# Kernel tuning notes

Hardware: AMD Instinct MI355X
Metric: run time of the kernel (lower is better)

The kernel has to match this reference:

```python
import jax, jax.numpy as jnp
import numpy as np
import itertools

KH = KW = 3
N_NZ = 5
K_OUT = 126  # C(9,5) -> all patterns, matches capped n_kernels
C_IN = 128


def setup_inputs() -> dict:
    key = jax.random.key(0)
    k1, k2 = jax.random.split(key)
    inputs = jax.random.normal(k1, (32, 112, 112, C_IN), dtype=jnp.float32)
    # sparse_kernel: (n_non_zero, in_channels, kernels), glorot-ish scale
    scale = (2.0 / (N_NZ * C_IN + K_OUT)) ** 0.5
    sparse_kernel = jax.random.normal(k2, (N_NZ, C_IN, K_OUT), dtype=jnp.float32) * scale
    bias = jnp.zeros((K_OUT,), dtype=jnp.float32)
    # deterministic unique sparsity patterns: all C(9,5) flat-position combos
    patterns = jnp.asarray(
        np.array(list(itertools.combinations(range(KH * KW), N_NZ)), dtype=np.int32)
    )  # (K_OUT, N_NZ) flat positions in [0, 9)
    return {"inputs": inputs, "sparse_kernel": sparse_kernel, "bias": bias, "patterns": patterns}


def reference(inputs, sparse_kernel, bias, patterns):
    k_out = patterns.shape[0]
    c_in = sparse_kernel.shape[1]
    kk = jnp.arange(k_out)[:, None]  # (K,1) broadcasts against (K,N)
    # scatter: dense_flat[pos, :, k] = sparse_kernel[n, :, k]
    updates = jnp.transpose(sparse_kernel, (2, 0, 1))  # (K, N, Cin)
    dense_flat = jnp.zeros((KH * KW, c_in, k_out), dtype=inputs.dtype)
    dense_flat = dense_flat.at[patterns, :, kk].set(updates)
    dense_kernel = dense_flat.reshape(KH, KW, c_in, k_out)
    out = jax.lax.conv_general_dilated(
        inputs, dense_kernel, window_strides=(1, 1), padding="SAME",
        dimension_numbers=("NHWC", "HWIO", "NHWC"))
    return jax.nn.relu(out + bias)
```

## Files before the change

### kernel.cpp

```cpp
#include <hip/hip_runtime.h>


typedef __attribute__((ext_vector_type(8))) __bf16 bf16x8;
typedef __attribute__((ext_vector_type(4))) float f32x4;

__device__ __forceinline__ unsigned short f2bf(float f) {
  unsigned int u = __builtin_bit_cast(unsigned int, f);
  u += 0x7fffu + ((u >> 16) & 1u);
  return (unsigned short)(u >> 16);
}

__global__ __launch_bounds__(256) void build_B(const float* __restrict__ sk,
                                               const int* __restrict__ patterns,
                                               unsigned short* __restrict__ Bws) {
  int idx = blockIdx.x * 256 + threadIdx.x;
  if (idx >= 9 * 128 * 128) return;
  int c = idx & 127;
  int n = (idx >> 7) & 127;
  int p = idx >> 14;
  float v = 0.f;
  if (n < 126) {
#pragma unroll
    for (int j = 0; j < 5; ++j)
      if (patterns[n * 5 + j] == p) v = sk[(j * 128 + c) * 126 + n];
  }
  int cc = c >> 5, cl = c & 31;
  Bws[(((p * 4 + cc) * 128) + n) * 32 + cl] = f2bf(v);
}

__global__ __launch_bounds__(256, 2) void conv_main(const float* __restrict__ in,
                                                    const unsigned short* __restrict__ Bws,
                                                    const float* __restrict__ bias,
                                                    float* __restrict__ out) {
  __shared__ unsigned short Alds[2 * 4 * 342 * 8];

  const int tid = threadIdx.x;
  const int bid = ((blockIdx.x & 7) * 448) + (blockIdx.x >> 3);
  const int nimg = bid / 112;
  const int y = bid - nimg * 112;
  const int lane = tid & 63;
  const int w = tid >> 6;
  const int quad = lane >> 4;
  const int lrow = lane & 15;

  const float* inb = in + (size_t)nimg * 112 * 112 * 128;

  f32x4 acc[7][2];
#pragma unroll
  for (int mt = 0; mt < 7; ++mt) { acc[mt][0] = (f32x4)0.f; acc[mt][1] = (f32x4)0.f; }

  float4 pf[11];
  auto loadA = [&](int cc) {
#pragma unroll
    for (int it = 0; it < 11; ++it) {
      int i = tid + it * 256;
      float4 v = make_float4(0.f, 0.f, 0.f, 0.f);
      if (i < 2736) {
        int c4 = i & 7;
        int rest = i >> 3;
        int r = rest / 114;
        int hx = rest - r * 114;
        int gy = y + r - 1;
        int gx = hx - 1;
        if ((unsigned)gy < 112u && (unsigned)gx < 112u)
          v = *(const float4*)(inb + ((size_t)gy * 112 + gx) * 128 + cc * 32 + c4 * 4);
      }
      pf[it] = v;
    }
  };
  auto writeA = [&](int b) {
#pragma unroll
    for (int it = 0; it < 11; ++it) {
      int i = tid + it * 256;
      if (i < 2736) {
        int c4 = i & 7;
        int rest = i >> 3;
        int q = c4 >> 1, h = c4 & 1;
        ushort4 s;
        s.x = f2bf(pf[it].x); s.y = f2bf(pf[it].y);
        s.z = f2bf(pf[it].z); s.w = f2bf(pf[it].w);
        *(ushort4*)&Alds[(((b * 4 + q) * 342) + rest) * 8 + h * 4] = s;
      }
    }
  };

  loadA(0);
  writeA(0);
  __syncthreads();

#pragma unroll 1
  for (int cc = 0; cc < 4; ++cc) {
    const int cur = cc & 1;
    bf16x8 b[9][2];
#pragma unroll
    for (int p = 0; p < 9; ++p)
#pragma unroll
      for (int j = 0; j < 2; ++j)
        b[p][j] = *(const bf16x8*)(Bws +
            (((size_t)(p * 4 + cc) * 128 + w * 32 + j * 16 + lrow) * 32 + quad * 8));

    if (cc < 3) loadA(cc + 1);

    const unsigned short* Ab = &Alds[(size_t)(cur * 4 + quad) * 2736];
#pragma unroll
    for (int p = 0; p < 9; ++p) {
      const int r = p / 3;
      const int px = p - r * 3;
      const int abase = (r * 114 + px + lrow) * 8;
#pragma unroll
      for (int mt = 0; mt < 7; ++mt) {
        bf16x8 a = *(const bf16x8*)&Ab[abase + mt * 128];
        acc[mt][0] = __builtin_amdgcn_mfma_f32_16x16x32_bf16(a, b[p][0], acc[mt][0], 0, 0, 0);
        acc[mt][1] = __builtin_amdgcn_mfma_f32_16x16x32_bf16(a, b[p][1], acc[mt][1], 0, 0, 0);
      }
    }

    if (cc < 3) {
      writeA(cur ^ 1);
      __syncthreads();
    }
  }

  const int k0 = w * 32 + lrow;
  const int k1 = k0 + 16;
  const float bv0 = bias[k0 < 126 ? k0 : 125];
  const float bv1 = bias[k1 < 126 ? k1 : 125];
  float* outrow = out + ((size_t)(nimg * 112 + y)) * 112 * 126;
#pragma unroll
  for (int mt = 0; mt < 7; ++mt) {
#pragma unroll
    for (int rg = 0; rg < 4; ++rg) {
      int x = mt * 16 + quad * 4 + rg;
      float* o = outrow + (size_t)x * 126;
      if (k0 < 126) { float v = acc[mt][0][rg] + bv0; o[k0] = v > 0.f ? v : 0.f; }
      if (k1 < 126) { float v = acc[mt][1][rg] + bv1; o[k1] = v > 0.f ? v : 0.f; }
    }
  }
}

extern "C" void kernel_launch(void* const* d_in, const int* in_sizes, int n_in,
                              void* d_out, int out_size, void* d_ws, size_t ws_size,
                              hipStream_t stream) {
  const float* in = (const float*)d_in[0];
  const float* sk = (const float*)d_in[1];
  const float* bias = (const float*)d_in[2];
  const int* patterns = (const int*)d_in[3];
  float* out = (float*)d_out;
  unsigned short* Bws = (unsigned short*)d_ws;

  build_B<<<dim3(576), dim3(256), 0, stream>>>(sk, patterns, Bws);
  conv_main<<<dim3(32 * 112), dim3(256), 0, stream>>>(in, Bws, bias, out);
}
```

Before: 433.7 us.

## Precompute padded bf16 input rows and stage them into LDS with async copies

Adds a pre-pass kernel that converts the fp32 NHWC input into padded, channel-chunk-blocked bf16 rows in workspace. The main conv kernel then fills LDS with direct global-to-LDS 16-byte async loads from three neighbour rows, using a zero row for image borders. This removes the per-block fp32 load, conversion and LDS write, and the kernel now targets three blocks per SM. The cost is an extra pass that reads the full input and writes a bf16 copy, plus a memset. The old kernel is kept as a fallback when the workspace is too small.

```diff
diff --git a/kernel.cpp b/kernel.cpp
--- a/kernel.cpp
+++ b/kernel.cpp
@@ -3,12 +3,25 @@
 
 typedef __attribute__((ext_vector_type(8))) __bf16 bf16x8;
 typedef __attribute__((ext_vector_type(4))) float f32x4;
+typedef __attribute__((ext_vector_type(8))) unsigned short ushort8;
 
 __device__ __forceinline__ unsigned short f2bf(float f) {
   unsigned int u = __builtin_bit_cast(unsigned int, f);
   u += 0x7fffu + ((u >> 16) & 1u);
   return (unsigned short)(u >> 16);
 }
+
+__device__ __forceinline__ void async_copy16(void* lds, const void* g) {
+  __builtin_amdgcn_global_load_lds(
+      (const __attribute__((address_space(1))) unsigned int*)g,
+      (__attribute__((address_space(3))) unsigned int*)lds, 16, 0, 0);
+}
+
+#define BWS_BYTES 294912
+#define ROW_BYTES 29184
+#define ROW_USH   14592
+#define AIN_BYTES (3584LL * ROW_BYTES)
+#define WS_NEED   ((size_t)BWS_BYTES + (size_t)AIN_BYTES + (size_t)ROW_BYTES)
 
 __global__ __launch_bounds__(256) void build_B(const float* __restrict__ sk,
                                                const int* __restrict__ patterns,
@@ -28,10 +41,127 @@
   Bws[(((p * 4 + cc) * 128) + n) * 32 + cl] = f2bf(v);
 }
 
-__global__ __launch_bounds__(256, 2) void conv_main(const float* __restrict__ in,
+__global__ __launch_bounds__(256) void conv_pre(const float* __restrict__ in,
+                                                unsigned short* __restrict__ Ain) {
+  const int bid = ((blockIdx.x & 7) * 448) + (blockIdx.x >> 3);
+  const float* inrow = in + (size_t)bid * 112 * 128;
+  unsigned short* orow = Ain + (size_t)bid * ROW_USH;
+  const int tid = threadIdx.x;
+#pragma unroll
+  for (int it = 0; it < 8; ++it) {
+    int j = tid + it * 256;
+    if (j < 1824) {
+      int px = j >> 4;
+      int ccq = j & 15;
+      int gx = px - 1;
+      ushort8 s = (ushort8)0;
+      if ((unsigned)gx < 112u) {
+        const float* p = inrow + (size_t)gx * 128 + ccq * 8;
+        float4 a = *(const float4*)p;
+        float4 b = *(const float4*)(p + 4);
+        s[0] = f2bf(a.x); s[1] = f2bf(a.y); s[2] = f2bf(a.z); s[3] = f2bf(a.w);
+        s[4] = f2bf(b.x); s[5] = f2bf(b.y); s[6] = f2bf(b.z); s[7] = f2bf(b.w);
+      }
+      int cc = ccq >> 2, q = ccq & 3;
+      *(ushort8*)(orow + cc * 3648 + q * 912 + px * 8) = s;
+    }
+  }
+}
+
+__global__ __launch_bounds__(256, 3) void conv_main(const unsigned short* __restrict__ Ain,
+                                                    const unsigned short* __restrict__ zp,
                                                     const unsigned short* __restrict__ Bws,
                                                     const float* __restrict__ bias,
                                                     float* __restrict__ out) {
+  __shared__ unsigned short Alds[2 * 1536 * 8];
+
+  const int tid = threadIdx.x;
+  const int bid = ((blockIdx.x & 7) * 448) + (blockIdx.x >> 3);
+  const int nimg = bid / 112;
+  const int y = bid - nimg * 112;
+  const int lane = tid & 63;
+  const int w = tid >> 6;
+  const int quad = lane >> 4;
+  const int lrow = lane & 15;
+
+  const unsigned short* rp0;
+  const unsigned short* rp1 = Ain + (size_t)bid * ROW_USH;
+  const unsigned short* rp2;
+  rp0 = (y > 0)   ? (rp1 - ROW_USH) : zp;
+  rp2 = (y < 111) ? (rp1 + ROW_USH) : zp;
+
+  f32x4 acc[7][2];
+#pragma unroll
+  for (int mt = 0; mt < 7; ++mt) { acc[mt][0] = (f32x4)0.f; acc[mt][1] = (f32x4)0.f; }
+
+  auto stage = [&](int cc, int buf) {
+    const unsigned short* c0 = rp0 + cc * 3648;
+    const unsigned short* c1 = rp1 + cc * 3648;
+    const unsigned short* c2 = rp2 + cc * 3648;
+#pragma unroll
+    for (int it = 0; it < 6; ++it) {
+      int i = tid + it * 256;
+      bool b1 = (i >= 456), b2 = (i >= 912);
+      int rem = i - (b2 ? 912 : (b1 ? 456 : 0));
+      const unsigned short* base = b2 ? c2 : (b1 ? c1 : c0);
+      const unsigned short* src = (i < 1368) ? (base + rem * 8) : zp;
+      async_copy16((void*)&Alds[(size_t)buf * 12288 + (size_t)i * 8], (const void*)src);
+    }
+  };
+
+  stage(0, 0);
+  __syncthreads();
+
+#pragma unroll 1
+  for (int cc = 0; cc < 4; ++cc) {
+    const int buf = cc & 1;
+    bf16x8 b[9][2];
+#pragma unroll
+    for (int p = 0; p < 9; ++p)
+#pragma unroll
+      for (int j = 0; j < 2; ++j)
+        b[p][j] = *(const bf16x8*)(Bws +
+            (((size_t)(p * 4 + cc) * 128 + w * 32 + j * 16 + lrow) * 32 + quad * 8));
+
+    if (cc < 3) stage(cc + 1, buf ^ 1);
+
+#pragma unroll
+    for (int p = 0; p < 9; ++p) {
+      const int r = p / 3;
+      const int px = p - r * 3;
+      const int abase = buf * 12288 + r * 3648 + quad * 912 + (px + lrow) * 8;
+#pragma unroll
+      for (int mt = 0; mt < 7; ++mt) {
+        bf16x8 a = *(const bf16x8*)&Alds[abase + mt * 128];
+        acc[mt][0] = __builtin_amdgcn_mfma_f32_16x16x32_bf16(a, b[p][0], acc[mt][0], 0, 0, 0);
+        acc[mt][1] = __builtin_amdgcn_mfma_f32_16x16x32_bf16(a, b[p][1], acc[mt][1], 0, 0, 0);
+      }
+    }
+
+    if (cc < 3) __syncthreads();
+  }
+
+  const int k0 = w * 32 + lrow;
+  const int k1 = k0 + 16;
+  const float bv0 = bias[k0 < 126 ? k0 : 125];
+  const float bv1 = bias[k1 < 126 ? k1 : 125];
+  float* outrow = out + (size_t)bid * 112 * 126;
+#pragma unroll
+  for (int mt = 0; mt < 7; ++mt) {
+#pragma unroll
+    for (int rg = 0; rg < 4; ++rg) {
+      int x = mt * 16 + quad * 4 + rg;
+      float* o = outrow + (size_t)x * 126;
+      if (k0 < 126) { float v = acc[mt][0][rg] + bv0; o[k0] = v > 0.f ? v : 0.f; }
+      if (k1 < 126) { float v = acc[mt][1][rg] + bv1; o[k1] = v > 0.f ? v : 0.f; }
+    }
+  }
+}
+
+__global__ __launch_bounds__(256, 2) void conv_main_fb(const float* __restrict__ in,
+                                                       const unsigned short* __restrict__ Bws,
+                                                       const float* __restrict__ bias,
+                                                       float* __restrict__ out) {
   __shared__ unsigned short Alds[2 * 4 * 342 * 8];
 
   const int tid = threadIdx.x;
@@ -125,7 +255,7 @@
   const int k1 = k0 + 16;
   const float bv0 = bias[k0 < 126 ? k0 : 125];
   const float bv1 = bias[k1 < 126 ? k1 : 125];
-  float* outrow = out + ((size_t)(nimg * 112 + y)) * 112 * 126;
+  float* outrow = out + (size_t)bid * 112 * 126;
 #pragma unroll
   for (int mt = 0; mt < 7; ++mt) {
 #pragma unroll
@@ -149,5 +279,14 @@
   unsigned short* Bws = (unsigned short*)d_ws;
 
   build_B<<<dim3(576), dim3(256), 0, stream>>>(sk, patterns, Bws);
-  conv_main<<<dim3(32 * 112), dim3(256), 0, stream>>>(in, Bws, bias, out);
-}
+
+  if (ws_size >= WS_NEED) {
+    unsigned short* Ain = (unsigned short*)((char*)d_ws + BWS_BYTES);
+    unsigned short* zp  = (unsigned short*)((char*)d_ws + BWS_BYTES + AIN_BYTES);
+    hipMemsetAsync(zp, 0, ROW_BYTES, stream);
+    conv_pre<<<dim3(32 * 112), dim3(256), 0, stream>>>(in, Ain);
+    conv_main<<<dim3(32 * 112), dim3(256), 0, stream>>>(Ain, zp, Bws, bias, out);
+  } else {
+    conv_main_fb<<<dim3(32 * 112), dim3(256), 0, stream>>>(in, Bws, bias, out);
+  }
+}
```

New measurement: 479.4 us. +10.5%, slower.
